# Optimization experiments

Measured on AMD Instinct MI355X. Metric: run time of the kernel, lower is better.

## Reference

```python
import jax, jax.numpy as jnp
from jax import lax
import numpy as np

D, H, W3 = 240, 144, 240
V = D * H * W3  # 8294400 voxels


def conv3d(x, w, padding, stride=(1, 1, 1), b=None):
    y = lax.conv_general_dilated(x, w, window_strides=stride, padding=padding,
                                 dimension_numbers=('NCDHW', 'OIDHW', 'NCDHW'))
    if b is not None:
        y = y + b[None, :, None, None, None]
    return y


def downsample_block(x, w):
    # conv(c_in -> c_out - c_in, k3 s2 p1) concat maxpool(2,2), then relu
    c = conv3d(x, w, [(1, 1)] * 3, stride=(2, 2, 2))
    p = lax.reduce_window(x, -jnp.inf, lax.max, (1, 1, 2, 2, 2), (1, 1, 2, 2, 2), 'VALID')
    return jax.nn.relu(jnp.concatenate([c, p], axis=1))


def bottleneck(x, w_in, w133, b133, w331, b331, w313, b313, w_out):
    y0 = jax.nn.relu(conv3d(x, w_in, [(0, 0)] * 3))
    y1 = jax.nn.relu(conv3d(y0, w133, [(0, 0), (1, 1), (1, 1)], b=b133))
    y2 = jax.nn.relu(conv3d(y1, w331, [(1, 1), (1, 1), (0, 0)], b=b331) + y1)
    y3 = jax.nn.relu(conv3d(y2, w313, [(1, 1), (0, 0), (1, 1)], b=b313) + y2 + y1)
    return jax.nn.relu(conv3d(y3, w_out, [(0, 0)] * 3) + x)  # residual=True


def project2d_3d(feature2d, depth_3d):
    b, c, h, w = feature2d.shape
    flat = feature2d.reshape(b, c, h * w)

    def one(feat, depth):  # feat [c, HW], depth [HW]
        # pixels with depth<=0 are redirected out of bounds and dropped (stay zero)
        idx = jnp.where(depth > 0, depth, V)
        out = jnp.zeros((V, feat.shape[0]), feat.dtype).at[idx].set(feat.T, mode='drop')
        return out.T  # [c, V]

    return jax.vmap(one)(flat, depth_3d).reshape(b, c, D, H, W3)


def setup_inputs() -> dict:
    key = jax.random.key(0)
    ks = jax.random.split(key, 20)
    f = lambda i, shape: jax.random.normal(ks[i], shape, jnp.float32) * 0.05
    return {
        'feature2d': jax.random.normal(ks[0], (1, 12, 480, 640), jnp.float32),
        'depth_3d': jax.random.randint(ks[1], (1, 480 * 640), 0, V),
        'w_ds1': f(2, (4, 12, 3, 3, 3)),
        'b1_w_in': f(3, (4, 16, 1, 1, 1)),
        'b1_w133': f(4, (4, 4, 1, 3, 3)), 'b1_b133': f(5, (4,)),
        'b1_w331': f(6, (4, 4, 3, 3, 1)), 'b1_b331': f(7, (4,)),
        'b1_w313': f(8, (4, 4, 3, 1, 3)), 'b1_b313': f(9, (4,)),
        'b1_w_out': f(10, (16, 4, 1, 1, 1)),
        'w_ds2': f(11, (16, 16, 3, 3, 3)),
        'b2_w_in': f(12, (8, 32, 1, 1, 1)),
        'b2_w133': f(13, (8, 8, 1, 3, 3)), 'b2_b133': f(14, (8,)),
        'b2_w331': f(15, (8, 8, 3, 3, 1)), 'b2_b331': f(16, (8,)),
        'b2_w313': f(17, (8, 8, 3, 1, 3)), 'b2_b313': f(18, (8,)),
        'b2_w_out': f(19, (32, 8, 1, 1, 1)),
    }


def reference(feature2d, depth_3d, w_ds1,
              b1_w_in, b1_w133, b1_b133, b1_w331, b1_b331, b1_w313, b1_b313, b1_w_out,
              w_ds2,
              b2_w_in, b2_w133, b2_b133, b2_w331, b2_b331, b2_w313, b2_b313, b2_w_out):
    # location == 'late'
    segres = project2d_3d(feature2d, depth_3d)  # [b,12,240,144,240]
    # AvgPool3d(k=3, p=1, s=1) with count_include_pad=True -> window sum / 27
    pool = lax.reduce_window(segres, 0.0, lax.add, (1, 1, 3, 3, 3), (1, 1, 1, 1, 1),
                             [(0, 0), (0, 0), (1, 1), (1, 1), (1, 1)]) / 27.0
    segres = segres + pool * (segres == 0).astype(segres.dtype)
    x = downsample_block(segres, w_ds1)  # [b,16,120,72,120]
    x = bottleneck(x, b1_w_in, b1_w133, b1_b133, b1_w331, b1_b331, b1_w313, b1_b313, b1_w_out)
    x = downsample_block(x, w_ds2)  # [b,32,60,36,60]
    x = bottleneck(x, b2_w_in, b2_w133, b2_b133, b2_w331, b2_b331, b2_w313, b2_b313, b2_w_out)
    return x
```

## Files before the change

kernel.cpp:

```cpp
#include <hip/hip_runtime.h>
#include <hip/hip_bf16.h>

typedef __hip_bfloat16 bf16;
typedef unsigned short u16;

static __device__ __forceinline__ float lo16(unsigned u) { return __uint_as_float(u << 16); }
static __device__ __forceinline__ float hi16(unsigned u) { return __uint_as_float(u & 0xFFFF0000u); }
static __device__ __forceinline__ unsigned f2u(float x) {
    unsigned u = __float_as_uint(x);
    return (u + 0x7FFFu + ((u >> 16) & 1u)) >> 16;
}
static __device__ __forceinline__ unsigned pack2(float a, float b) {
    return f2u(a) | (f2u(b) << 16);
}

constexpr int D0 = 240, H0 = 144, W0 = 240;
constexpr int V  = D0 * H0 * W0;
constexpr int NPIX = 480 * 640;
constexpr int D1 = 120, H1 = 72, W1 = 120;
constexpr int N1 = D1 * H1 * W1;
constexpr int D2 = 60, H2 = 36, W2 = 60;
constexpr int N2 = D2 * H2 * W2;

constexpr size_t GRP_U16  = (size_t)V * 4;
constexpr size_t GRP_BYTES = GRP_U16 * sizeof(u16);
constexpr size_t SEG_BYTES = 3 * GRP_BYTES;
constexpr size_t WIN_BYTES = (size_t)V * sizeof(unsigned);
constexpr int ZCHUNKS = (int)((SEG_BYTES + WIN_BYTES) / 16);

__global__ void __launch_bounds__(256) kz_zero16(uint4* __restrict__ p, int nchunks) {
    int i = blockIdx.x * 256 + threadIdx.x;
    if (i >= nchunks) return;
    p[i] = make_uint4(0u, 0u, 0u, 0u);
}

__global__ void __launch_bounds__(256) kz_scatter_win(const int* __restrict__ depth,
                                                      unsigned* __restrict__ winner) {
    int p = blockIdx.x * 256 + threadIdx.x;
    if (p >= NPIX) return;
    int d = depth[p];
    if (d > 0 && d < V) atomicMax(&winner[d], (unsigned)(p + 1));
}

__global__ void __launch_bounds__(256) kz_scatter_write(const int* __restrict__ depth,
                                                        const unsigned* __restrict__ winner,
                                                        const float* __restrict__ feat,
                                                        u16* __restrict__ seg) {
    int p = blockIdx.x * 256 + threadIdx.x;
    if (p >= NPIX) return;
    int d = depth[p];
    if (d > 0 && d < V && winner[d] == (unsigned)(p + 1)) {
#pragma unroll
        for (int g = 0; g < 3; ++g) {
            uint2 val;
            val.x = pack2(feat[(4 * g + 0) * NPIX + p], feat[(4 * g + 1) * NPIX + p]);
            val.y = pack2(feat[(4 * g + 2) * NPIX + p], feat[(4 * g + 3) * NPIX + p]);
            *(uint2*)(seg + g * GRP_U16 + (size_t)d * 4) = val;
        }
    }
}

constexpr int FTW = 120;
constexpr int FROWS = 36;

__global__ void __launch_bounds__(256) kz_fillL(const u16* __restrict__ rb,
                                                u16* __restrict__ fb) {
    __shared__ u16 S[FROWS * FTW * 4];
    int bid = blockIdx.x;
    int wt = bid & 1;
    int t1 = bid >> 1;
    int ht = t1 % 36;
    int dt = t1 / 36;
    int d0 = dt * 4, h0 = ht * 4, w0 = wt * 120;
    int tid = threadIdx.x;

    for (int tt = tid; tt < FROWS * 60; tt += 256) {
        int hr = tt / 60;
        int pt = tt - hr * 60;
        int w = w0 + 2 * pt;
        int d = d0 - 1 + hr / 6;
        int h = h0 - 1 + hr % 6;
        uint4 O = make_uint4(0u, 0u, 0u, 0u);
        if (d >= 0 && d < D0 && h >= 0 && h < H0) {
            const u16* rp = rb + (size_t)((d * H0 + h) * W0 + w) * 4;
            uint4 X = *(const uint4*)(rp);
            float x0[4] = {lo16(X.x), hi16(X.x), lo16(X.y), hi16(X.y)};
            float x1[4] = {lo16(X.z), hi16(X.z), lo16(X.w), hi16(X.w)};
            float l[4] = {0.f, 0.f, 0.f, 0.f}, rr[4] = {0.f, 0.f, 0.f, 0.f};
            if (w > 0) {
                uint2 L = *(const uint2*)(rp - 4);
                l[0] = lo16(L.x); l[1] = hi16(L.x); l[2] = lo16(L.y); l[3] = hi16(L.y);
            }
            if (w < 238) {
                uint2 R = *(const uint2*)(rp + 8);
                rr[0] = lo16(R.x); rr[1] = hi16(R.x); rr[2] = lo16(R.y); rr[3] = hi16(R.y);
            }
            O.x = pack2(l[0] + x0[0] + x1[0], l[1] + x0[1] + x1[1]);
            O.y = pack2(l[2] + x0[2] + x1[2], l[3] + x0[3] + x1[3]);
            O.z = pack2(x0[0] + x1[0] + rr[0], x0[1] + x1[1] + rr[1]);
            O.w = pack2(x0[2] + x1[2] + rr[2], x0[3] + x1[3] + rr[3]);
        }
        *(uint4*)(S + ((size_t)hr * FTW + 2 * pt) * 4) = O;
    }
    __syncthreads();

    for (int ot = tid; ot < 16 * 60; ot += 256) {
        int orr = ot / 60;
        int pt = ot - orr * 60;
        int w = w0 + 2 * pt;
        int di = orr >> 2, hi_ = orr & 3;
        int d = d0 + di, h = h0 + hi_;
        float s[8] = {0.f, 0.f, 0.f, 0.f, 0.f, 0.f, 0.f, 0.f};
#pragma unroll
        for (int dd = 0; dd < 3; ++dd) {
#pragma unroll
            for (int dh = 0; dh < 3; ++dh) {
                int hr = (di + dd) * 6 + (hi_ + dh);
                uint4 T = *(const uint4*)(S + ((size_t)hr * FTW + 2 * pt) * 4);
                s[0] += lo16(T.x); s[1] += hi16(T.x); s[2] += lo16(T.y); s[3] += hi16(T.y);
                s[4] += lo16(T.z); s[5] += hi16(T.z); s[6] += lo16(T.w); s[7] += hi16(T.w);
            }
        }
        size_t gi = (size_t)((d * H0 + h) * W0 + w) * 4;
        uint4 Rv = *(const uint4*)(rb + gi);
        constexpr float inv27 = 1.0f / 27.0f;
        uint4 Ov;
        Ov.x = ((Rv.x & 0x7FFFu) ? (Rv.x & 0xFFFFu) : f2u(s[0] * inv27))
             | ((((Rv.x >> 16) & 0x7FFFu) ? (Rv.x >> 16) : f2u(s[1] * inv27)) << 16);
        Ov.y = ((Rv.y & 0x7FFFu) ? (Rv.y & 0xFFFFu) : f2u(s[2] * inv27))
             | ((((Rv.y >> 16) & 0x7FFFu) ? (Rv.y >> 16) : f2u(s[3] * inv27)) << 16);
        Ov.z = ((Rv.z & 0x7FFFu) ? (Rv.z & 0xFFFFu) : f2u(s[4] * inv27))
             | ((((Rv.z >> 16) & 0x7FFFu) ? (Rv.z >> 16) : f2u(s[5] * inv27)) << 16);
        Ov.w = ((Rv.w & 0x7FFFu) ? (Rv.w & 0xFFFFu) : f2u(s[6] * inv27))
             | ((((Rv.w >> 16) & 0x7FFFu) ? (Rv.w >> 16) : f2u(s[7] * inv27)) << 16);
        *(uint4*)(fb + gi) = Ov;
    }
}

__global__ void __launch_bounds__(256) kz_ds1(const u16* __restrict__ f0g,
                                              const u16* __restrict__ f1g,
                                              const u16* __restrict__ f2g,
                                              const float* __restrict__ w,
                                              float* __restrict__ x1i) {
    __shared__ float wl[4 * 12 * 27];
    __shared__ float pool[12 * 256];
    for (int t = threadIdx.x; t < 4 * 12 * 27; t += 256) wl[t] = w[t];
    __syncthreads();
    int tid = threadIdx.x;
    int o = blockIdx.x * 256 + tid;
    int wo = o % W1;
    int t  = o / W1;
    int ho = t % H1;
    int d0 = t / H1;
    float acc[4] = {0.f, 0.f, 0.f, 0.f};
#pragma unroll 1
    for (int g = 0; g < 3; ++g) {
        const u16* base = (g == 0) ? f0g : ((g == 1) ? f1g : f2g);
        const float* wg = wl + (4 * g) * 27;
        float mx0 = -1e30f, mx1 = -1e30f, mx2 = -1e30f, mx3 = -1e30f;
#pragma unroll 1
        for (int kd = 0; kd < 3; ++kd) {
            int d2 = 2 * d0 - 1 + kd;
            bool dv = (d2 >= 0 && d2 < D0);
#pragma unroll
            for (int kh = 0; kh < 3; ++kh) {
                int h2 = 2 * ho - 1 + kh;
                bool rvv = dv && (h2 >= 0 && h2 < H0);
                float a0 = 0.f, a1 = 0.f, a2 = 0.f, a3 = 0.f;
                float b0 = 0.f, b1 = 0.f, b2 = 0.f, b3 = 0.f;
                float c0 = 0.f, c1 = 0.f, c2 = 0.f, c3 = 0.f;
                if (rvv) {
                    size_t r2 = (size_t)((d2 * H0 + h2) * W0 + 2 * wo);
                    uint4 AB = *(const uint4*)(base + r2 * 4);
                    b0 = lo16(AB.x); b1 = hi16(AB.x); b2 = lo16(AB.y); b3 = hi16(AB.y);
                    c0 = lo16(AB.z); c1 = hi16(AB.z); c2 = lo16(AB.w); c3 = hi16(AB.w);
                    if (wo > 0) {
                        uint2 P = *(const uint2*)(base + (r2 - 1) * 4);
                        a0 = lo16(P.x); a1 = hi16(P.x); a2 = lo16(P.y); a3 = hi16(P.y);
                    }
                }
                const float* wk = wg + kd * 9 + kh * 3;
#pragma unroll
                for (int m = 0; m < 4; ++m) {
                    const float* wm = wk + m * 324;
                    acc[m] += a0 * wm[0]  + b0 * wm[1]  + c0 * wm[2]
                            + a1 * wm[27] + b1 * wm[28] + c1 * wm[29]
                            + a2 * wm[54] + b2 * wm[55] + c2 * wm[56]
                            + a3 * wm[81] + b3 * wm[82] + c3 * wm[83];
                }
                if (kd >= 1 && kh >= 1) {
                    mx0 = fmaxf(mx0, fmaxf(b0, c0));
                    mx1 = fmaxf(mx1, fmaxf(b1, c1));
                    mx2 = fmaxf(mx2, fmaxf(b2, c2));
                    mx3 = fmaxf(mx3, fmaxf(b3, c3));
                }
            }
        }
        pool[(4 * g + 0) * 256 + tid] = fmaxf(mx0, 0.f);
        pool[(4 * g + 1) * 256 + tid] = fmaxf(mx1, 0.f);
        pool[(4 * g + 2) * 256 + tid] = fmaxf(mx2, 0.f);
        pool[(4 * g + 3) * 256 + tid] = fmaxf(mx3, 0.f);
    }
    float* xo = x1i + (size_t)o * 16;
    *(float4*)(xo)      = make_float4(fmaxf(acc[0], 0.f), fmaxf(acc[1], 0.f),
                                      fmaxf(acc[2], 0.f), fmaxf(acc[3], 0.f));
    *(float4*)(xo + 4)  = make_float4(pool[0 * 256 + tid], pool[1 * 256 + tid],
                                      pool[2 * 256 + tid], pool[3 * 256 + tid]);
    *(float4*)(xo + 8)  = make_float4(pool[4 * 256 + tid], pool[5 * 256 + tid],
                                      pool[6 * 256 + tid], pool[7 * 256 + tid]);
    *(float4*)(xo + 12) = make_float4(pool[8 * 256 + tid], pool[9 * 256 + tid],
                                      pool[10 * 256 + tid], pool[11 * 256 + tid]);
}

__global__ void __launch_bounds__(256) kz_pw16to4i(const float* __restrict__ in,
                                                   const float* __restrict__ w,
                                                   float* __restrict__ out) {
    __shared__ float wl[64];
    if (threadIdx.x < 64) wl[threadIdx.x] = w[threadIdx.x];
    __syncthreads();
    int o = blockIdx.x * 256 + threadIdx.x;
    const float* ip = in + (size_t)o * 16;
    float4 A = *(const float4*)(ip);
    float4 B = *(const float4*)(ip + 4);
    float4 C = *(const float4*)(ip + 8);
    float4 D = *(const float4*)(ip + 12);
    float r[4];
#pragma unroll
    for (int m = 0; m < 4; ++m) {
        const float* wm = wl + m * 16;
        r[m] = A.x * wm[0] + A.y * wm[1] + A.z * wm[2] + A.w * wm[3]
             + B.x * wm[4] + B.y * wm[5] + B.z * wm[6] + B.w * wm[7]
             + C.x * wm[8] + C.y * wm[9] + C.z * wm[10] + C.w * wm[11]
             + D.x * wm[12] + D.y * wm[13] + D.z * wm[14] + D.w * wm[15];
    }
    *(float4*)(out + (size_t)o * 4) = make_float4(fmaxf(r[0], 0.f), fmaxf(r[1], 0.f),
                                                  fmaxf(r[2], 0.f), fmaxf(r[3], 0.f));
}

template <int KD, int KH, int KW, int NADD>
__global__ void __launch_bounds__(256) kz_bconv4i(const float* __restrict__ in,
                                                  const float* __restrict__ w,
                                                  const float* __restrict__ b,
                                                  const float* __restrict__ add1,
                                                  const float* __restrict__ add2,
                                                  float* __restrict__ out) {
    constexpr int S = KD * KH * KW;
    __shared__ float wl[16 * S];
    __shared__ float bl[4];
    for (int t = threadIdx.x; t < 16 * S; t += 256) wl[t] = w[t];
    if (threadIdx.x < 4) bl[threadIdx.x] = b[threadIdx.x];
    __syncthreads();
    int o = blockIdx.x * 256 + threadIdx.x;
    int wo = o % W1;
    int t  = o / W1;
    int ho = t % H1;
    int d0 = t / H1;
    float a0 = bl[0], a1 = bl[1], a2 = bl[2], a3 = bl[3];
#pragma unroll
    for (int kd = 0; kd < KD; ++kd) {
        int d2 = d0 + kd - KD / 2;
        if (KD > 1 && (d2 < 0 || d2 >= D1)) continue;
#pragma unroll
        for (int kh = 0; kh < KH; ++kh) {
            int h2 = ho + kh - KH / 2;
            if (KH > 1 && (h2 < 0 || h2 >= H1)) continue;
#pragma unroll
            for (int kw = 0; kw < KW; ++kw) {
                int w2 = wo + kw - KW / 2;
                if (KW > 1 && (w2 < 0 || w2 >= W1)) continue;
                float4 v = *(const float4*)(in + (size_t)((d2 * H1 + h2) * W1 + w2) * 4);
                int tap = (kd * KH + kh) * KW + kw;
                const float* wt = wl + tap;
                a0 += v.x * wt[0 * S] + v.y * wt[1 * S] + v.z * wt[2 * S] + v.w * wt[3 * S];
                a1 += v.x * wt[4 * S] + v.y * wt[5 * S] + v.z * wt[6 * S] + v.w * wt[7 * S];
                a2 += v.x * wt[8 * S] + v.y * wt[9 * S] + v.z * wt[10 * S] + v.w * wt[11 * S];
                a3 += v.x * wt[12 * S] + v.y * wt[13 * S] + v.z * wt[14 * S] + v.w * wt[15 * S];
            }
        }
    }
    if (NADD >= 1) {
        float4 r1 = *(const float4*)(add1 + (size_t)o * 4);
        a0 += r1.x; a1 += r1.y; a2 += r1.z; a3 += r1.w;
    }
    if (NADD >= 2) {
        float4 r2 = *(const float4*)(add2 + (size_t)o * 4);
        a0 += r2.x; a1 += r2.y; a2 += r2.z; a3 += r2.w;
    }
    *(float4*)(out + (size_t)o * 4) = make_float4(fmaxf(a0, 0.f), fmaxf(a1, 0.f),
                                                  fmaxf(a2, 0.f), fmaxf(a3, 0.f));
}

__global__ void __launch_bounds__(256) kz_bconv4i_pw(const float* __restrict__ in,
                                                     const float* __restrict__ w,
                                                     const float* __restrict__ b,
                                                     const float* __restrict__ add1,
                                                     const float* __restrict__ add2,
                                                     const float* __restrict__ wp,
                                                     const float* __restrict__ x1i,
                                                     float* __restrict__ out) {
    constexpr int S = 9;
    __shared__ float wl[16 * S];
    __shared__ float bl[4];
    __shared__ float wpl[64];
    for (int t = threadIdx.x; t < 16 * S; t += 256) wl[t] = w[t];
    if (threadIdx.x < 4) bl[threadIdx.x] = b[threadIdx.x];
    if (threadIdx.x < 64) wpl[threadIdx.x] = wp[threadIdx.x];
    __syncthreads();
    int o = blockIdx.x * 256 + threadIdx.x;
    int wo = o % W1;
    int t  = o / W1;
    int ho = t % H1;
    int d0 = t / H1;
    float a0 = bl[0], a1 = bl[1], a2 = bl[2], a3 = bl[3];
#pragma unroll
    for (int kd = 0; kd < 3; ++kd) {
        int d2 = d0 + kd - 1;
        if (d2 < 0 || d2 >= D1) continue;
#pragma unroll
        for (int kw = 0; kw < 3; ++kw) {
            int w2 = wo + kw - 1;
            if (w2 < 0 || w2 >= W1) continue;
            float4 v = *(const float4*)(in + (size_t)((d2 * H1 + ho) * W1 + w2) * 4);
            int tap = kd * 3 + kw;
            const float* wt = wl + tap;
            a0 += v.x * wt[0 * S] + v.y * wt[1 * S] + v.z * wt[2 * S] + v.w * wt[3 * S];
            a1 += v.x * wt[4 * S] + v.y * wt[5 * S] + v.z * wt[6 * S] + v.w * wt[7 * S];
            a2 += v.x * wt[8 * S] + v.y * wt[9 * S] + v.z * wt[10 * S] + v.w * wt[11 * S];
            a3 += v.x * wt[12 * S] + v.y * wt[13 * S] + v.z * wt[14 * S] + v.w * wt[15 * S];
        }
    }
    float4 r1 = *(const float4*)(add1 + (size_t)o * 4);
    float4 r2 = *(const float4*)(add2 + (size_t)o * 4);
    float y0 = fmaxf(a0 + r1.x + r2.x, 0.f);
    float y1 = fmaxf(a1 + r1.y + r2.y, 0.f);
    float y2 = fmaxf(a2 + r1.z + r2.z, 0.f);
    float y3 = fmaxf(a3 + r1.w + r2.w, 0.f);
    const float* rp = x1i + (size_t)o * 16;
    float4 R0 = *(const float4*)(rp);
    float4 R1 = *(const float4*)(rp + 4);
    float4 R2 = *(const float4*)(rp + 8);
    float4 R3 = *(const float4*)(rp + 12);
    float rr[16] = {R0.x, R0.y, R0.z, R0.w, R1.x, R1.y, R1.z, R1.w,
                    R2.x, R2.y, R2.z, R2.w, R3.x, R3.y, R3.z, R3.w};
#pragma unroll
    for (int m = 0; m < 16; ++m) {
        const float* wm = wpl + m * 4;
        float r = y0 * wm[0] + y1 * wm[1] + y2 * wm[2] + y3 * wm[3] + rr[m];
        out[(size_t)m * N1 + o] = fmaxf(r, 0.f);
    }
}

__global__ void __launch_bounds__(256) kz_ds2f(const float* __restrict__ in,
                                               const float* __restrict__ w,
                                               const float* __restrict__ wz,
                                               float* __restrict__ out,
                                               float* __restrict__ z0i) {
    __shared__ float wl[16 * 16 * 27];
    __shared__ float wzl[256];
    for (int t = threadIdx.x; t < 16 * 16 * 27; t += 256) wl[t] = w[t];
    if (threadIdx.x < 256) wzl[threadIdx.x] = wz[threadIdx.x];
    __syncthreads();
    int o = blockIdx.x * 256 + threadIdx.x;
    if (o >= N2) return;
    int wo = o % W2;
    int t  = o / W2;
    int ho = t % H2;
    int d0 = t / H2;
    float acc[16];
    float zacc[8];
#pragma unroll
    for (int m = 0; m < 16; ++m) acc[m] = 0.f;
#pragma unroll
    for (int m = 0; m < 8; ++m) zacc[m] = 0.f;
#pragma unroll 1
    for (int ci = 0; ci < 16; ++ci) {
        const float* base = in + ci * N1;
        const float* wci = wl + ci * 27;
        float mx = -1e30f;
#pragma unroll 1
        for (int kd = 0; kd < 3; ++kd) {
            int d2 = 2 * d0 - 1 + kd;
            bool dv = (d2 >= 0 && d2 < D1);
#pragma unroll
            for (int kh = 0; kh < 3; ++kh) {
                int h2 = 2 * ho - 1 + kh;
                bool rvv = dv && (h2 >= 0 && h2 < H1);
                float vm1 = 0.f, v0 = 0.f, v1 = 0.f;
                if (rvv) {
                    int r2 = (d2 * H1 + h2) * W1 + 2 * wo;
                    float2 pb = *(const float2*)(base + r2);
                    v0 = pb.x; v1 = pb.y;
                    if (wo > 0) {
                        float2 pa = *(const float2*)(base + r2 - 2);
                        vm1 = pa.y;
                    }
                }
                const float* wk = wci + kd * 9 + kh * 3;
#pragma unroll
                for (int m = 0; m < 16; ++m)
                    acc[m] += vm1 * wk[m * 432] + v0 * wk[m * 432 + 1] + v1 * wk[m * 432 + 2];
                if (kd >= 1 && kh >= 1) mx = fmaxf(mx, fmaxf(v0, v1));
            }
        }
        float pl = fmaxf(mx, 0.f);
        out[(16 + ci) * N2 + o] = pl;
#pragma unroll
        for (int m = 0; m < 8; ++m) zacc[m] += wzl[m * 32 + 16 + ci] * pl;
    }
#pragma unroll
    for (int j = 0; j < 16; ++j) {
        float cj = fmaxf(acc[j], 0.f);
        out[j * N2 + o] = cj;
#pragma unroll
        for (int m = 0; m < 8; ++m) zacc[m] += wzl[m * 32 + j] * cj;
    }
    float* op = z0i + (size_t)o * 8;
    *(float4*)(op)     = make_float4(fmaxf(zacc[0], 0.f), fmaxf(zacc[1], 0.f),
                                     fmaxf(zacc[2], 0.f), fmaxf(zacc[3], 0.f));
    *(float4*)(op + 4) = make_float4(fmaxf(zacc[4], 0.f), fmaxf(zacc[5], 0.f),
                                     fmaxf(zacc[6], 0.f), fmaxf(zacc[7], 0.f));
}

template <int KD, int KH, int KW, int NADD>
__global__ void __launch_bounds__(256) kz_bconv8i(const float* __restrict__ in,
                                                  const float* __restrict__ w,
                                                  const float* __restrict__ b,
                                                  const float* __restrict__ add1,
                                                  const float* __restrict__ add2,
                                                  float* __restrict__ out) {
    constexpr int S = KD * KH * KW;
    __shared__ float wl[64 * S];
    __shared__ float bl[8];
    for (int t = threadIdx.x; t < 64 * S; t += 256) wl[t] = w[t];
    if (threadIdx.x < 8) bl[threadIdx.x] = b[threadIdx.x];
    __syncthreads();
    int o = blockIdx.x * 256 + threadIdx.x;
    if (o >= N2) return;
    int wo = o % W2;
    int t  = o / W2;
    int ho = t % H2;
    int d0 = t / H2;
    float acc[8];
#pragma unroll
    for (int m = 0; m < 8; ++m) acc[m] = bl[m];
#pragma unroll
    for (int kd = 0; kd < KD; ++kd) {
        int d2 = d0 + kd - KD / 2;
        if (KD > 1 && (d2 < 0 || d2 >= D2)) continue;
#pragma unroll
        for (int kh = 0; kh < KH; ++kh) {
            int h2 = ho + kh - KH / 2;
            if (KH > 1 && (h2 < 0 || h2 >= H2)) continue;
#pragma unroll
            for (int kw = 0; kw < KW; ++kw) {
                int w2 = wo + kw - KW / 2;
                if (KW > 1 && (w2 < 0 || w2 >= W2)) continue;
                const float* vp = in + (size_t)((d2 * H2 + h2) * W2 + w2) * 8;
                float4 v0 = *(const float4*)(vp);
                float4 v1 = *(const float4*)(vp + 4);
                int tap = (kd * KH + kh) * KW + kw;
                const float* wt = wl + tap;
#pragma unroll
                for (int m = 0; m < 8; ++m) {
                    const float* wm = wt + m * 8 * S;
                    acc[m] += v0.x * wm[0] + v0.y * wm[S] + v0.z * wm[2 * S] + v0.w * wm[3 * S]
                            + v1.x * wm[4 * S] + v1.y * wm[5 * S] + v1.z * wm[6 * S] + v1.w * wm[7 * S];
                }
            }
        }
    }
    if (NADD >= 1) {
        const float* ap = add1 + (size_t)o * 8;
        float4 r0 = *(const float4*)(ap), r1 = *(const float4*)(ap + 4);
        acc[0] += r0.x; acc[1] += r0.y; acc[2] += r0.z; acc[3] += r0.w;
        acc[4] += r1.x; acc[5] += r1.y; acc[6] += r1.z; acc[7] += r1.w;
    }
    if (NADD >= 2) {
        const float* ap = add2 + (size_t)o * 8;
        float4 r0 = *(const float4*)(ap), r1 = *(const float4*)(ap + 4);
        acc[0] += r0.x; acc[1] += r0.y; acc[2] += r0.z; acc[3] += r0.w;
        acc[4] += r1.x; acc[5] += r1.y; acc[6] += r1.z; acc[7] += r1.w;
    }
    float* op = out + (size_t)o * 8;
    *(float4*)(op)     = make_float4(fmaxf(acc[0], 0.f), fmaxf(acc[1], 0.f),
                                     fmaxf(acc[2], 0.f), fmaxf(acc[3], 0.f));
    *(float4*)(op + 4) = make_float4(fmaxf(acc[4], 0.f), fmaxf(acc[5], 0.f),
                                     fmaxf(acc[6], 0.f), fmaxf(acc[7], 0.f));
}

__global__ void __launch_bounds__(256) kz_bconv8i_pw(const float* __restrict__ in,
                                                     const float* __restrict__ w,
                                                     const float* __restrict__ b,
                                                     const float* __restrict__ add1,
                                                     const float* __restrict__ add2,
                                                     const float* __restrict__ wp,
                                                     const float* __restrict__ resp,
                                                     float* __restrict__ out) {
    constexpr int S = 9;
    __shared__ float wl[64 * S];
    __shared__ float bl[8];
    __shared__ float wpl[256];
    for (int t = threadIdx.x; t < 64 * S; t += 256) wl[t] = w[t];
    if (threadIdx.x < 8) bl[threadIdx.x] = b[threadIdx.x];
    if (threadIdx.x < 256) wpl[threadIdx.x] = wp[threadIdx.x];
    __syncthreads();
    int o = blockIdx.x * 256 + threadIdx.x;
    if (o >= N2) return;
    int wo = o % W2;
    int t  = o / W2;
    int ho = t % H2;
    int d0 = t / H2;
    float acc[8];
#pragma unroll
    for (int m = 0; m < 8; ++m) acc[m] = bl[m];
#pragma unroll
    for (int kd = 0; kd < 3; ++kd) {
        int d2 = d0 + kd - 1;
        if (d2 < 0 || d2 >= D2) continue;
#pragma unroll
        for (int kw = 0; kw < 3; ++kw) {
            int w2 = wo + kw - 1;
            if (w2 < 0 || w2 >= W2) continue;
            const float* vp = in + (size_t)((d2 * H2 + ho) * W2 + w2) * 8;
            float4 v0 = *(const float4*)(vp);
            float4 v1 = *(const float4*)(vp + 4);
            int tap = kd * 3 + kw;
            const float* wt = wl + tap;
#pragma unroll
            for (int m = 0; m < 8; ++m) {
                const float* wm = wt + m * 8 * S;
                acc[m] += v0.x * wm[0] + v0.y * wm[S] + v0.z * wm[2 * S] + v0.w * wm[3 * S]
                        + v1.x * wm[4 * S] + v1.y * wm[5 * S] + v1.z * wm[6 * S] + v1.w * wm[7 * S];
            }
        }
    }
    {
        const float* ap = add1 + (size_t)o * 8;
        float4 r0 = *(const float4*)(ap), r1 = *(const float4*)(ap + 4);
        acc[0] += r0.x; acc[1] += r0.y; acc[2] += r0.z; acc[3] += r0.w;
        acc[4] += r1.x; acc[5] += r1.y; acc[6] += r1.z; acc[7] += r1.w;
    }
    {
        const float* ap = add2 + (size_t)o * 8;
        float4 r0 = *(const float4*)(ap), r1 = *(const float4*)(ap + 4);
        acc[0] += r0.x; acc[1] += r0.y; acc[2] += r0.z; acc[3] += r0.w;
        acc[4] += r1.x; acc[5] += r1.y; acc[6] += r1.z; acc[7] += r1.w;
    }
#pragma unroll
    for (int m = 0; m < 8; ++m) acc[m] = fmaxf(acc[m], 0.f);
#pragma unroll
    for (int m = 0; m < 32; ++m) {
        const float* wm = wpl + m * 8;
        float r = acc[0] * wm[0] + acc[1] * wm[1] + acc[2] * wm[2] + acc[3] * wm[3]
                + acc[4] * wm[4] + acc[5] * wm[5] + acc[6] * wm[6] + acc[7] * wm[7];
        r += resp[(size_t)m * N2 + o];
        out[(size_t)m * N2 + o] = fmaxf(r, 0.f);
    }
}

extern "C" void kernel_launch(void* const* d_in, const int* in_sizes, int n_in,
                              void* d_out, int out_size, void* d_ws, size_t ws_size,
                              hipStream_t stream) {
    const float* feat   = (const float*)d_in[0];
    const int*   depth  = (const int*)d_in[1];
    const float* w_ds1  = (const float*)d_in[2];
    const float* b1_win = (const float*)d_in[3];
    const float* b1w133 = (const float*)d_in[4];
    const float* b1b133 = (const float*)d_in[5];
    const float* b1w331 = (const float*)d_in[6];
    const float* b1b331 = (const float*)d_in[7];
    const float* b1w313 = (const float*)d_in[8];
    const float* b1b313 = (const float*)d_in[9];
    const float* b1wout = (const float*)d_in[10];
    const float* w_ds2  = (const float*)d_in[11];
    const float* b2_win = (const float*)d_in[12];
    const float* b2w133 = (const float*)d_in[13];
    const float* b2b133 = (const float*)d_in[14];
    const float* b2w331 = (const float*)d_in[15];
    const float* b2b331 = (const float*)d_in[16];
    const float* b2w313 = (const float*)d_in[17];
    const float* b2b313 = (const float*)d_in[18];
    const float* b2wout = (const float*)d_in[19];

    char* base = (char*)d_ws;

    u16* raw0 = (u16*)base;
    u16* raw1 = (u16*)(base + GRP_BYTES);
    u16* raw2 = (u16*)(base + 2 * GRP_BYTES);
    unsigned* winner = (unsigned*)(base + SEG_BYTES);
    u16* fil0 = (u16*)(base + SEG_BYTES);
    u16* fil1 = (u16*)base;
    u16* fil2 = (u16*)(base + GRP_BYTES);
    float* x1i = (float*)(base + 2 * GRP_BYTES);
    float* y0i = (float*)base;
    float* y1i = y0i + 4 * N1;
    float* y2i = y1i + 4 * N1;
    float* x1b = (float*)(base + SEG_BYTES);
    float* x2  = (float*)base;
    float* z0i = x2 + 32 * N2;
    float* z1i = z0i + 8 * N2;
    float* z2i = z1i + 8 * N2;

    float* out = (float*)d_out;

    kz_zero16<<<ZCHUNKS / 256, 256, 0, stream>>>((uint4*)base, ZCHUNKS);

    kz_scatter_win  <<<NPIX / 256, 256, 0, stream>>>(depth, winner);
    kz_scatter_write<<<NPIX / 256, 256, 0, stream>>>(depth, winner, feat, raw0);

    kz_fillL<<<4320, 256, 0, stream>>>(raw0, fil0);
    kz_fillL<<<4320, 256, 0, stream>>>(raw1, fil1);
    kz_fillL<<<4320, 256, 0, stream>>>(raw2, fil2);

    kz_ds1<<<N1 / 256, 256, 0, stream>>>(fil0, fil1, fil2, w_ds1, x1i);

    kz_pw16to4i<<<N1 / 256, 256, 0, stream>>>(x1i, b1_win, y0i);
    kz_bconv4i<1, 3, 3, 0><<<N1 / 256, 256, 0, stream>>>(y0i, b1w133, b1b133, nullptr, nullptr, y1i);
    kz_bconv4i<3, 3, 1, 1><<<N1 / 256, 256, 0, stream>>>(y1i, b1w331, b1b331, y1i, nullptr, y2i);
    kz_bconv4i_pw<<<N1 / 256, 256, 0, stream>>>(y2i, b1w313, b1b313, y2i, y1i, b1wout, x1i, x1b);

    kz_ds2f<<<(N2 + 255) / 256, 256, 0, stream>>>(x1b, w_ds2, b2_win, x2, z0i);

    kz_bconv8i<1, 3, 3, 0><<<(N2 + 255) / 256, 256, 0, stream>>>(z0i, b2w133, b2b133, nullptr, nullptr, z1i);
    kz_bconv8i<3, 3, 1, 1><<<(N2 + 255) / 256, 256, 0, stream>>>(z1i, b2w331, b2b331, z1i, nullptr, z2i);
    kz_bconv8i_pw<<<(N2 + 255) / 256, 256, 0, stream>>>(z2i, b2w313, b2b313, z2i, z1i, b2wout, x2, out);

    (void)in_sizes; (void)n_in; (void)out_size; (void)ws_size;
}
```

Before: 734.6 us.

## Skip zeroing the scattered grid by gating reads with the winner map

When the workspace is large enough, only the winner array is zeroed instead of the full three-group scatter buffer plus the winner array. The fill kernels read the winner map and mask raw values at voxels that received no pixel, so uninitialised data is never used. The first filled group moves to a separate region so it does not overwrite the winner map. This removes most of the memory-set traffic, at the cost of extra winner reads in each of the three fill passes.

```diff
diff --git a/kernel.cpp b/kernel.cpp
--- a/kernel.cpp
+++ b/kernel.cpp
@@ -26,7 +26,9 @@
 constexpr size_t GRP_BYTES = GRP_U16 * sizeof(u16);
 constexpr size_t SEG_BYTES = 3 * GRP_BYTES;
 constexpr size_t WIN_BYTES = (size_t)V * sizeof(unsigned);
-constexpr int ZCHUNKS = (int)((SEG_BYTES + WIN_BYTES) / 16);
+constexpr int ZCHUNKS  = (int)((SEG_BYTES + WIN_BYTES) / 16);
+constexpr int WCHUNKS  = (int)(WIN_BYTES / 16);
+constexpr size_t BIG_WS = SEG_BYTES + WIN_BYTES + GRP_BYTES;
 
 __global__ void __launch_bounds__(256) kz_zero16(uint4* __restrict__ p, int nchunks) {
     int i = blockIdx.x * 256 + threadIdx.x;
@@ -63,7 +65,9 @@
 constexpr int FTW = 120;
 constexpr int FROWS = 36;
 
+template <bool GATED>
 __global__ void __launch_bounds__(256) kz_fillL(const u16* __restrict__ rb,
+                                                const unsigned* __restrict__ win,
                                                 u16* __restrict__ fb) {
     __shared__ u16 S[FROWS * FTW * 4];
     int bid = blockIdx.x;
@@ -82,17 +86,25 @@
         int h = h0 - 1 + hr % 6;
         uint4 O = make_uint4(0u, 0u, 0u, 0u);
         if (d >= 0 && d < D0 && h >= 0 && h < H0) {
-            const u16* rp = rb + (size_t)((d * H0 + h) * W0 + w) * 4;
+            size_t row = (size_t)(d * H0 + h) * W0;
+            const u16* rp = rb + (row + w) * 4;
             uint4 X = *(const uint4*)(rp);
+            if (GATED) {
+                uint2 WN = *(const uint2*)(win + row + w);
+                if (WN.x == 0u) { X.x = 0u; X.y = 0u; }
+                if (WN.y == 0u) { X.z = 0u; X.w = 0u; }
+            }
             float x0[4] = {lo16(X.x), hi16(X.x), lo16(X.y), hi16(X.y)};
             float x1[4] = {lo16(X.z), hi16(X.z), lo16(X.w), hi16(X.w)};
             float l[4] = {0.f, 0.f, 0.f, 0.f}, rr[4] = {0.f, 0.f, 0.f, 0.f};
             if (w > 0) {
                 uint2 L = *(const uint2*)(rp - 4);
+                if (GATED && win[row + w - 1] == 0u) { L.x = 0u; L.y = 0u; }
                 l[0] = lo16(L.x); l[1] = hi16(L.x); l[2] = lo16(L.y); l[3] = hi16(L.y);
             }
             if (w < 238) {
                 uint2 R = *(const uint2*)(rp + 8);
+                if (GATED && win[row + w + 2] == 0u) { R.x = 0u; R.y = 0u; }
                 rr[0] = lo16(R.x); rr[1] = hi16(R.x); rr[2] = lo16(R.y); rr[3] = hi16(R.y);
             }
             O.x = pack2(l[0] + x0[0] + x1[0], l[1] + x0[1] + x1[1]);
@@ -121,8 +133,14 @@
                 s[4] += lo16(T.z); s[5] += hi16(T.z); s[6] += lo16(T.w); s[7] += hi16(T.w);
             }
         }
-        size_t gi = (size_t)((d * H0 + h) * W0 + w) * 4;
+        size_t row = (size_t)(d * H0 + h) * W0;
+        size_t gi = (row + w) * 4;
         uint4 Rv = *(const uint4*)(rb + gi);
+        if (GATED) {
+            uint2 WN = *(const uint2*)(win + row + w);
+            if (WN.x == 0u) { Rv.x = 0u; Rv.y = 0u; }
+            if (WN.y == 0u) { Rv.z = 0u; Rv.w = 0u; }
+        }
         constexpr float inv27 = 1.0f / 27.0f;
         uint4 Ov;
         Ov.x = ((Rv.x & 0x7FFFu) ? (Rv.x & 0xFFFFu) : f2u(s[0] * inv27))
@@ -583,12 +601,13 @@
     const float* b2wout = (const float*)d_in[19];
 
     char* base = (char*)d_ws;
+    const bool bigws = (ws_size >= BIG_WS);
 
     u16* raw0 = (u16*)base;
     u16* raw1 = (u16*)(base + GRP_BYTES);
     u16* raw2 = (u16*)(base + 2 * GRP_BYTES);
     unsigned* winner = (unsigned*)(base + SEG_BYTES);
-    u16* fil0 = (u16*)(base + SEG_BYTES);
+    u16* fil0 = bigws ? (u16*)(base + SEG_BYTES + WIN_BYTES) : (u16*)(base + SEG_BYTES);
     u16* fil1 = (u16*)base;
     u16* fil2 = (u16*)(base + GRP_BYTES);
     float* x1i = (float*)(base + 2 * GRP_BYTES);
@@ -603,14 +622,24 @@
 
     float* out = (float*)d_out;
 
-    kz_zero16<<<ZCHUNKS / 256, 256, 0, stream>>>((uint4*)base, ZCHUNKS);
+    if (bigws) {
+        kz_zero16<<<WCHUNKS / 256, 256, 0, stream>>>((uint4*)winner, WCHUNKS);
+    } else {
+        kz_zero16<<<ZCHUNKS / 256, 256, 0, stream>>>((uint4*)base, ZCHUNKS);
+    }
 
     kz_scatter_win  <<<NPIX / 256, 256, 0, stream>>>(depth, winner);
     kz_scatter_write<<<NPIX / 256, 256, 0, stream>>>(depth, winner, feat, raw0);
 
-    kz_fillL<<<4320, 256, 0, stream>>>(raw0, fil0);
-    kz_fillL<<<4320, 256, 0, stream>>>(raw1, fil1);
-    kz_fillL<<<4320, 256, 0, stream>>>(raw2, fil2);
+    if (bigws) {
+        kz_fillL<true><<<4320, 256, 0, stream>>>(raw0, winner, fil0);
+        kz_fillL<true><<<4320, 256, 0, stream>>>(raw1, winner, fil1);
+        kz_fillL<true><<<4320, 256, 0, stream>>>(raw2, winner, fil2);
+    } else {
+        kz_fillL<false><<<4320, 256, 0, stream>>>(raw0, nullptr, fil0);
+        kz_fillL<false><<<4320, 256, 0, stream>>>(raw1, nullptr, fil1);
+        kz_fillL<false><<<4320, 256, 0, stream>>>(raw2, nullptr, fil2);
+    }
 
     kz_ds1<<<N1 / 256, 256, 0, stream>>>(fil0, fil1, fil2, w_ds1, x1i);
 
@@ -625,5 +654,5 @@
     kz_bconv8i<3, 3, 1, 1><<<(N2 + 255) / 256, 256, 0, stream>>>(z1i, b2w331, b2b331, z1i, nullptr, z2i);
     kz_bconv8i_pw<<<(N2 + 255) / 256, 256, 0, stream>>>(z2i, b2w313, b2b313, z2i, z1i, b2wout, x2, out);
 
-    (void)in_sizes; (void)n_in; (void)out_size; (void)ws_size;
-}
+    (void)in_sizes; (void)n_in; (void)out_size;
+}
```

Measured after the change: 732.3 us. About the same (-0.3%).

## Replace full scatter-buffer zeroing with a winner-derived occupancy gate mask

Applied to the files above, without the earlier changes.

Stops zero-filling the three large bf16 scatter buffers and zeroes only the winner array. A new kernel packs the winner array into a per-voxel byte mask stored in the output buffer as scratch. The fill kernels then treat unset voxels as zero by consulting the mask, so stale buffer contents are ignored. This trades roughly 200MB of memset writes for an extra small kernel and byte-mask reads inside the fill stencil.

```diff
diff --git a/kernel.cpp b/kernel.cpp
--- a/kernel.cpp
+++ b/kernel.cpp
@@ -3,6 +3,7 @@
 
 typedef __hip_bfloat16 bf16;
 typedef unsigned short u16;
+typedef unsigned char u8;
 
 static __device__ __forceinline__ float lo16(unsigned u) { return __uint_as_float(u << 16); }
 static __device__ __forceinline__ float hi16(unsigned u) { return __uint_as_float(u & 0xFFFF0000u); }
@@ -26,7 +27,7 @@
 constexpr size_t GRP_BYTES = GRP_U16 * sizeof(u16);
 constexpr size_t SEG_BYTES = 3 * GRP_BYTES;
 constexpr size_t WIN_BYTES = (size_t)V * sizeof(unsigned);
-constexpr int ZCHUNKS = (int)((SEG_BYTES + WIN_BYTES) / 16);
+constexpr int WCHUNKS  = (int)(WIN_BYTES / 16);
 
 __global__ void __launch_bounds__(256) kz_zero16(uint4* __restrict__ p, int nchunks) {
     int i = blockIdx.x * 256 + threadIdx.x;
@@ -60,10 +61,23 @@
     }
 }
 
+__global__ void __launch_bounds__(256) kz_gate(const uint4* __restrict__ win,
+                                               uint4* __restrict__ gate) {
+    int i = blockIdx.x * 256 + threadIdx.x;
+    const uint4* wp = win + (size_t)i * 4;
+    uint4 a = wp[0], b = wp[1], c = wp[2], d = wp[3];
+    unsigned r0 = (a.x ? 1u : 0u) | (a.y ? 0x100u : 0u) | (a.z ? 0x10000u : 0u) | (a.w ? 0x1000000u : 0u);
+    unsigned r1 = (b.x ? 1u : 0u) | (b.y ? 0x100u : 0u) | (b.z ? 0x10000u : 0u) | (b.w ? 0x1000000u : 0u);
+    unsigned r2 = (c.x ? 1u : 0u) | (c.y ? 0x100u : 0u) | (c.z ? 0x10000u : 0u) | (c.w ? 0x1000000u : 0u);
+    unsigned r3 = (d.x ? 1u : 0u) | (d.y ? 0x100u : 0u) | (d.z ? 0x10000u : 0u) | (d.w ? 0x1000000u : 0u);
+    gate[i] = make_uint4(r0, r1, r2, r3);
+}
+
 constexpr int FTW = 120;
 constexpr int FROWS = 36;
 
 __global__ void __launch_bounds__(256) kz_fillL(const u16* __restrict__ rb,
+                                                const u8* __restrict__ gate,
                                                 u16* __restrict__ fb) {
     __shared__ u16 S[FROWS * FTW * 4];
     int bid = blockIdx.x;
@@ -82,16 +96,20 @@
         int h = h0 - 1 + hr % 6;
         uint4 O = make_uint4(0u, 0u, 0u, 0u);
         if (d >= 0 && d < D0 && h >= 0 && h < H0) {
-            const u16* rp = rb + (size_t)((d * H0 + h) * W0 + w) * 4;
+            size_t row = (size_t)(d * H0 + h) * W0;
+            size_t gi = row + w;
+            const u16* rp = rb + gi * 4;
             uint4 X = *(const uint4*)(rp);
+            if (gate[gi] == 0)     { X.x = 0u; X.y = 0u; }
+            if (gate[gi + 1] == 0) { X.z = 0u; X.w = 0u; }
             float x0[4] = {lo16(X.x), hi16(X.x), lo16(X.y), hi16(X.y)};
             float x1[4] = {lo16(X.z), hi16(X.z), lo16(X.w), hi16(X.w)};
             float l[4] = {0.f, 0.f, 0.f, 0.f}, rr[4] = {0.f, 0.f, 0.f, 0.f};
-            if (w > 0) {
+            if (w > 0 && gate[gi - 1] != 0) {
                 uint2 L = *(const uint2*)(rp - 4);
                 l[0] = lo16(L.x); l[1] = hi16(L.x); l[2] = lo16(L.y); l[3] = hi16(L.y);
             }
-            if (w < 238) {
+            if (w < 238 && gate[gi + 2] != 0) {
                 uint2 R = *(const uint2*)(rp + 8);
                 rr[0] = lo16(R.x); rr[1] = hi16(R.x); rr[2] = lo16(R.y); rr[3] = hi16(R.y);
             }
@@ -121,8 +139,11 @@
                 s[4] += lo16(T.z); s[5] += hi16(T.z); s[6] += lo16(T.w); s[7] += hi16(T.w);
             }
         }
-        size_t gi = (size_t)((d * H0 + h) * W0 + w) * 4;
-        uint4 Rv = *(const uint4*)(rb + gi);
+        size_t row = (size_t)(d * H0 + h) * W0;
+        size_t gi = row + w;
+        uint4 Rv = *(const uint4*)(rb + gi * 4);
+        if (gate[gi] == 0)     { Rv.x = 0u; Rv.y = 0u; }
+        if (gate[gi + 1] == 0) { Rv.z = 0u; Rv.w = 0u; }
         constexpr float inv27 = 1.0f / 27.0f;
         uint4 Ov;
         Ov.x = ((Rv.x & 0x7FFFu) ? (Rv.x & 0xFFFFu) : f2u(s[0] * inv27))
@@ -133,7 +154,7 @@
              | ((((Rv.z >> 16) & 0x7FFFu) ? (Rv.z >> 16) : f2u(s[5] * inv27)) << 16);
         Ov.w = ((Rv.w & 0x7FFFu) ? (Rv.w & 0xFFFFu) : f2u(s[6] * inv27))
              | ((((Rv.w >> 16) & 0x7FFFu) ? (Rv.w >> 16) : f2u(s[7] * inv27)) << 16);
-        *(uint4*)(fb + gi) = Ov;
+        *(uint4*)(fb + gi * 4) = Ov;
     }
 }
 
@@ -602,15 +623,18 @@
     float* z2i = z1i + 8 * N2;
 
     float* out = (float*)d_out;
-
-    kz_zero16<<<ZCHUNKS / 256, 256, 0, stream>>>((uint4*)base, ZCHUNKS);
+    u8* gate = (u8*)d_out;
+
+    kz_zero16<<<WCHUNKS / 256, 256, 0, stream>>>((uint4*)winner, WCHUNKS);
 
     kz_scatter_win  <<<NPIX / 256, 256, 0, stream>>>(depth, winner);
     kz_scatter_write<<<NPIX / 256, 256, 0, stream>>>(depth, winner, feat, raw0);
 
-    kz_fillL<<<4320, 256, 0, stream>>>(raw0, fil0);
-    kz_fillL<<<4320, 256, 0, stream>>>(raw1, fil1);
-    kz_fillL<<<4320, 256, 0, stream>>>(raw2, fil2);
+    kz_gate<<<(V / 16) / 256, 256, 0, stream>>>((const uint4*)winner, (uint4*)gate);
+
+    kz_fillL<<<4320, 256, 0, stream>>>(raw0, gate, fil0);
+    kz_fillL<<<4320, 256, 0, stream>>>(raw1, gate, fil1);
+    kz_fillL<<<4320, 256, 0, stream>>>(raw2, gate, fil2);
 
     kz_ds1<<<N1 / 256, 256, 0, stream>>>(fil0, fil1, fil2, w_ds1, x1i);
 
```

New measurement: 791.6 us. 7.8% more time.
